# Kernel tuning notes

Hardware: AMD Instinct MI355X
Metric: run time of the kernel (lower is better)

## Reference

```python
import jax, jax.numpy as jnp
import numpy as np

N = 100000
E = 1600000
IN_C, HID_C, OUT_C = 128, 64, 16


def setup_inputs() -> dict:
    key = jax.random.key(0)
    k1, k2, k3, k4, k5 = jax.random.split(key, 5)
    x = jax.random.normal(k1, (N, IN_C), dtype=jnp.float32)
    edge_index = jax.random.randint(k2, (2, E), 0, N, dtype=jnp.int64)
    edge_weight = jax.random.uniform(k3, (E,), dtype=jnp.float32)
    # GCNConv weights (Glorot init, bias=False)
    W1 = jax.random.normal(k4, (IN_C, HID_C), dtype=jnp.float32) * (1.0 / np.sqrt(IN_C))
    W2 = jax.random.normal(k5, (HID_C, OUT_C), dtype=jnp.float32) * (1.0 / np.sqrt(HID_C))
    return {"x": x, "edge_index": edge_index, "edge_weight": edge_weight, "W1": W1, "W2": W2}


def _gcn_norm(edge_index, edge_weight, num_nodes):
    # add self loops with weight 1 (PyG gcn_norm with add_self_loops=True)
    loop = jnp.arange(num_nodes, dtype=edge_index.dtype)
    row = jnp.concatenate([edge_index[0], loop])
    col = jnpp_concat = jnp.concatenate([edge_index[1], loop])
    w = jnp.concatenate([edge_weight, jnp.ones((num_nodes,), edge_weight.dtype)])
    deg = jax.ops.segment_sum(w, col, num_segments=num_nodes)
    dinv = jnp.where(deg > 0, jax.lax.rsqrt(deg), 0.0)
    norm = dinv[row] * w * dinv[col]
    return row, col, norm


def _gcn_conv(x, W, row, col, norm, num_nodes):
    h = x @ W                              # [N, C_out] dense projection
    msg = h[row] * norm[:, None]           # gather + scale per edge
    return jax.ops.segment_sum(msg, col, num_segments=num_nodes)  # scatter-add at dst


def reference(x, edge_index, edge_weight, W1, W2):
    num_nodes = x.shape[0]
    row, col, norm = _gcn_norm(edge_index, edge_weight, num_nodes)
    h = _gcn_conv(x, W1, row, col, norm, num_nodes)
    h = jax.nn.relu(h)  # dropout_rate == 0 / eval -> identity
    h = _gcn_conv(h, W2, row, col, norm, num_nodes)
    return jax.nn.log_softmax(h, axis=1)
```

## Files before the change

### kernel.cpp

```cpp
#include <hip/hip_runtime.h>
#include <hip/hip_fp16.h>
#include <math.h>

constexpr int IN_C = 128, HID_C = 64, OUT_C = 16;
constexpr int BSH = 7;
constexpr int BCAP = 2560;
constexpr int REC_PT = BCAP / 256;
constexpr int TILE = 4096;
constexpr float WSC = 33554432.0f;

using f16x8 = __attribute__((ext_vector_type(8))) _Float16;
using f32x4 = __attribute__((ext_vector_type(4))) float;

__global__ __launch_bounds__(256) void k_hist(const int* __restrict__ col, int* __restrict__ histG,
                                              int E, int nb) {
  __shared__ int h[1024];
  int t = threadIdx.x, tile = blockIdx.x;
  for (int i = t; i < nb; i += 256) h[i] = 0;
  __syncthreads();
  int base = tile * TILE;
#pragma unroll
  for (int u = 0; u < TILE / 256; ++u) {
    int e = base + u * 256 + t;
    if (e < E) atomicAdd(&h[col[e] >> BSH], 1);
  }
  __syncthreads();
  for (int i = t; i < nb; i += 256) histG[(size_t)tile * nb + i] = h[i];
}

__global__ __launch_bounds__(256) void k_cscan(int* __restrict__ histG, int* __restrict__ btot,
                                               int T, int nb) {
  int b = blockIdx.x, t = threadIdx.x;
  __shared__ int s[512];
  int i0 = t, i1 = t + 256;
  s[i0] = (i0 < T) ? histG[(size_t)i0 * nb + b] : 0;
  s[i1] = (i1 < T) ? histG[(size_t)i1 * nb + b] : 0;
  __syncthreads();
  int c0 = s[i0], c1 = s[i1];
  for (int off = 1; off < 512; off <<= 1) {
    int a0 = (i0 >= off) ? s[i0 - off] : 0;
    int a1 = (i1 >= off) ? s[i1 - off] : 0;
    __syncthreads();
    s[i0] += a0; s[i1] += a1;
    __syncthreads();
  }
  if (i0 < T) histG[(size_t)i0 * nb + b] = s[i0] - c0;
  if (i1 < T) histG[(size_t)i1 * nb + b] = s[i1] - c1;
  if (t == 0) btot[b] = s[511];
}

__global__ __launch_bounds__(256) void k_scat2(const int* __restrict__ row, const int* __restrict__ col,
                                               const float* __restrict__ w, const int* __restrict__ histG,
                                               uint2* __restrict__ rec, int E, int nb) {
  __shared__ int soff[1024];
  int t = threadIdx.x, tile = blockIdx.x;
  for (int i = t; i < nb; i += 256) soff[i] = histG[(size_t)tile * nb + i];
  __syncthreads();
  int base = tile * TILE;
#pragma unroll
  for (int u = 0; u < TILE / 256; ++u) {
    int e = base + u * 256 + t;
    if (e < E) {
      int r = row[e], d = col[e];
      int b = d >> BSH;
      unsigned lo = (unsigned)(d & ((1 << BSH) - 1));
      unsigned wf = __float2uint_rn(w[e] * WSC);
      if (wf > 33554431u) wf = 33554431u;
      int slot = atomicAdd(&soff[b], 1);
      if (slot < BCAP)
        rec[(size_t)b * BCAP + slot] = make_uint2((unsigned)r, (lo << 25) | wf);
    }
  }
}

__global__ __launch_bounds__(256) void k_buck(const int* __restrict__ btot, const uint2* __restrict__ rec,
                                              int2* __restrict__ pairs, int* __restrict__ ptrg,
                                              int* __restrict__ cntg, float* __restrict__ dinvg,
                                              int n) {
  int b = blockIdx.x;
  int t = threadIdx.x;
  int cnt = btot[b];
  if (cnt > BCAP) cnt = BCAP;
  __shared__ int lcnt[128];
  __shared__ float lws[128];
  __shared__ int lptr[128];
  if (t < 128) { lcnt[t] = 0; lws[t] = 0.f; }
  __syncthreads();
  uint2 rv[REC_PT];
  int rk[REC_PT];
#pragma unroll
  for (int u = 0; u < REC_PT; ++u) {
    int i = u * 256 + t;
    if (i < cnt) {
      uint2 v = rec[(size_t)b * BCAP + i];
      rv[u] = v;
      int lo = v.y >> 25;
      rk[u] = atomicAdd(&lcnt[lo], 1);
      atomicAdd(&lws[lo], (float)(v.y & 0x1FFFFFFu) * (1.0f / WSC));
    }
  }
  __syncthreads();
  if (t < 128) lptr[t] = lcnt[t];
  __syncthreads();
  for (int off = 1; off < 128; off <<= 1) {
    int v = (t < 128 && t >= off) ? lptr[t - off] : 0;
    __syncthreads();
    if (t < 128 && t >= off) lptr[t] += v;
    __syncthreads();
  }
  if (t < 128) {
    int d = (b << BSH) + t;
    if (d < n) {
      ptrg[d] = b * BCAP + lptr[t] - lcnt[t];
      cntg[d] = lcnt[t];
      dinvg[d] = rsqrtf(1.0f + lws[t]);
    }
  }
#pragma unroll
  for (int u = 0; u < REC_PT; ++u) {
    int i = u * 256 + t;
    if (i < cnt) {
      uint2 v = rv[u];
      int lo = v.y >> 25;
      float wv = (float)(v.y & 0x1FFFFFFu) * (1.0f / WSC);
      pairs[(size_t)b * BCAP + (lptr[lo] - lcnt[lo]) + rk[u]] = make_int2((int)v.x, __float_as_int(wv));
    }
  }
}

__global__ __launch_bounds__(256) void k_gemm1(const float* __restrict__ x, const float* __restrict__ W1,
                                               const float* __restrict__ dinv,
                                               __half* __restrict__ h1h, int n) {
  __shared__ _Float16 w1t[HID_C][IN_C];
  int t = threadIdx.x;
  for (int i = t; i < IN_C * HID_C / 4; i += 256) {
    float4 v = ((const float4*)W1)[i];
    int k = (i * 4) / HID_C;
    int c = (i * 4) % HID_C;
    w1t[c + 0][k] = (_Float16)v.x;
    w1t[c + 1][k] = (_Float16)v.y;
    w1t[c + 2][k] = (_Float16)v.z;
    w1t[c + 3][k] = (_Float16)v.w;
  }
  __syncthreads();
  int wave = t >> 6, lane = t & 63;
  int row0 = (blockIdx.x * 4 + wave) * 16;
  if (row0 >= n) return;
  int lrow = lane & 15, lkg = lane >> 4;
  bool rvalid = (row0 + lrow) < n;
  const float* xr = x + (size_t)(row0 + lrow) * IN_C;
  f32x4 acc[4];
#pragma unroll
  for (int cg = 0; cg < 4; ++cg) acc[cg] = (f32x4){0.f, 0.f, 0.f, 0.f};
#pragma unroll
  for (int ks = 0; ks < 4; ++ks) {
    int k0 = ks * 32 + lkg * 8;
    f16x8 a;
    if (rvalid) {
      float4 u0 = *(const float4*)&xr[k0];
      float4 u1 = *(const float4*)&xr[k0 + 4];
      a[0] = (_Float16)u0.x; a[1] = (_Float16)u0.y; a[2] = (_Float16)u0.z; a[3] = (_Float16)u0.w;
      a[4] = (_Float16)u1.x; a[5] = (_Float16)u1.y; a[6] = (_Float16)u1.z; a[7] = (_Float16)u1.w;
    } else {
#pragma unroll
      for (int j = 0; j < 8; ++j) a[j] = (_Float16)0.f;
    }
#pragma unroll
    for (int cg = 0; cg < 4; ++cg) {
      f16x8 bfrag = *(const f16x8*)&w1t[cg * 16 + lrow][k0];
      acc[cg] = __builtin_amdgcn_mfma_f32_16x16x32_f16(a, bfrag, acc[cg], 0, 0, 0);
    }
  }
  float dv[4];
#pragma unroll
  for (int r = 0; r < 4; ++r) {
    int gr = row0 + lkg * 4 + r;
    dv[r] = (gr < n) ? dinv[gr] : 0.f;
  }
#pragma unroll
  for (int cg = 0; cg < 4; ++cg) {
#pragma unroll
    for (int r = 0; r < 4; ++r) {
      int gr = row0 + lkg * 4 + r;
      if (gr < n)
        h1h[(size_t)gr * HID_C + cg * 16 + lrow] = __float2half_rn(dv[r] * acc[cg][r]);
    }
  }
}

__global__ __launch_bounds__(256) void k_agg1f(const int* __restrict__ ptr, const int* __restrict__ cnt,
                                               const int2* __restrict__ pairs, const float* __restrict__ dinv,
                                               const __half* __restrict__ h1h, const float* __restrict__ W2,
                                               __half* __restrict__ h2h, int n) {
  __shared__ float w2s[HID_C * OUT_C];
  __shared__ float s[4][68];
  int t = threadIdx.x;
  ((float4*)w2s)[t] = ((const float4*)W2)[t];
  int wv = t >> 6, lane = t & 63;
  int d = blockIdx.x * 4 + wv;
  if (d < n) {
    d = __builtin_amdgcn_readfirstlane(d);
    int k = ptr[d], end = k + cnt[d];
    float dd = dinv[d];
    float acc = __half2float(h1h[(size_t)d * HID_C + lane]);
    for (; k + 8 <= end; k += 8) {
      int2 p[8];
      float v[8];
#pragma unroll
      for (int u = 0; u < 8; ++u) p[u] = pairs[k + u];
#pragma unroll
      for (int u = 0; u < 8; ++u)
        v[u] = __half2float(h1h[(size_t)p[u].x * HID_C + lane]);
#pragma unroll
      for (int u = 0; u < 8; ++u) acc = fmaf(__int_as_float(p[u].y), v[u], acc);
    }
    if (k + 4 <= end) {
      int2 p[4];
      float v[4];
#pragma unroll
      for (int u = 0; u < 4; ++u) p[u] = pairs[k + u];
#pragma unroll
      for (int u = 0; u < 4; ++u)
        v[u] = __half2float(h1h[(size_t)p[u].x * HID_C + lane]);
#pragma unroll
      for (int u = 0; u < 4; ++u) acc = fmaf(__int_as_float(p[u].y), v[u], acc);
      k += 4;
    }
    for (; k < end; ++k) {
      int2 p = pairs[k];
      acc = fmaf(__int_as_float(p.y), __half2float(h1h[(size_t)p.x * HID_C + lane]), acc);
    }
    s[wv][lane] = fmaxf(dd * acc, 0.f);
  } else {
    s[wv][lane] = 0.f;
  }
  __syncthreads();
  if (t < 64) {
    int nl = t >> 4, j = t & 15;
    int dn = blockIdx.x * 4 + nl;
    if (dn < n) {
      float a2 = 0.f;
#pragma unroll
      for (int c = 0; c < HID_C; ++c) a2 = fmaf(s[nl][c], w2s[c * OUT_C + j], a2);
      h2h[(size_t)dn * OUT_C + j] = __float2half_rn(dinv[dn] * a2);
    }
  }
}

__global__ __launch_bounds__(256) void k_agg2(const int* __restrict__ ptr, const int* __restrict__ cnt,
                                              const int2* __restrict__ pairs, const float* __restrict__ dinv,
                                              const __half* __restrict__ h2h, float* __restrict__ out, int n) {
  int t = threadIdx.x;
  int d = blockIdx.x * 16 + (t >> 4);
  if (d >= n) return;
  int j = t & 15;
  int k = ptr[d], end = k + cnt[d];
  float dd = dinv[d];
  float acc = __half2float(h2h[(size_t)d * OUT_C + j]);
  for (; k + 8 <= end; k += 8) {
    int2 p[8];
    float v[8];
#pragma unroll
    for (int u = 0; u < 8; ++u) p[u] = pairs[k + u];
#pragma unroll
    for (int u = 0; u < 8; ++u)
      v[u] = __half2float(h2h[(size_t)p[u].x * OUT_C + j]);
#pragma unroll
    for (int u = 0; u < 8; ++u) acc = fmaf(__int_as_float(p[u].y), v[u], acc);
  }
  if (k + 4 <= end) {
    int2 p[4];
    float v[4];
#pragma unroll
    for (int u = 0; u < 4; ++u) p[u] = pairs[k + u];
#pragma unroll
    for (int u = 0; u < 4; ++u)
      v[u] = __half2float(h2h[(size_t)p[u].x * OUT_C + j]);
#pragma unroll
    for (int u = 0; u < 4; ++u) acc = fmaf(__int_as_float(p[u].y), v[u], acc);
    k += 4;
  }
  for (; k < end; ++k) {
    int2 p = pairs[k];
    acc = fmaf(__int_as_float(p.y), __half2float(h2h[(size_t)p.x * OUT_C + j]), acc);
  }
  float lg = dd * acc;
  float mx = lg;
#pragma unroll
  for (int off = 8; off; off >>= 1) mx = fmaxf(mx, __shfl_xor(mx, off, 16));
  float sm = expf(lg - mx);
#pragma unroll
  for (int off = 8; off; off >>= 1) sm += __shfl_xor(sm, off, 16);
  out[(size_t)d * OUT_C + j] = lg - mx - logf(sm);
}

extern "C" void kernel_launch(void* const* d_in, const int* in_sizes, int n_in,
                              void* d_out, int out_size, void* d_ws, size_t ws_size,
                              hipStream_t stream) {
  const float* x  = (const float*)d_in[0];
  const int*   ei = (const int*)d_in[1];
  const float* ew = (const float*)d_in[2];
  const float* W1 = (const float*)d_in[3];
  const float* W2 = (const float*)d_in[4];
  const int N = in_sizes[0] / IN_C;
  const int E = in_sizes[2];
  const int* row = ei;
  const int* col = ei + E;
  float* out = (float*)d_out;
  const int NBUK = (N + (1 << BSH) - 1) >> BSH;
  const int T = (E + TILE - 1) / TILE;

  char* p = (char*)d_ws;
  int2*  pairs= (int2*)p;             p += (size_t)NBUK * BCAP * 8;
  int*   ptr  = (int*)p;              p += (size_t)N * 4;
  int*   cnt  = (int*)p;              p += (size_t)N * 4;
  float* dinv = (float*)p;            p += (size_t)N * 4;
  int*   histG= (int*)p;              p += (size_t)T * NBUK * 4;
  int*   btot = (int*)p;              p += (size_t)NBUK * 4;
  char*  uni  = p;                    p += (size_t)N * HID_C * 4;
  uint2* rec  = (uint2*)uni;
  __half* h1h = (__half*)uni;
  __half* h2h = (__half*)(uni + (size_t)N * HID_C * 2);

  dim3 b(256);
  k_hist <<<T, b, 0, stream>>>(col, histG, E, NBUK);
  k_cscan<<<NBUK, b, 0, stream>>>(histG, btot, T, NBUK);
  k_scat2<<<T, b, 0, stream>>>(row, col, ew, histG, rec, E, NBUK);
  k_buck <<<NBUK, b, 0, stream>>>(btot, rec, pairs, ptr, cnt, dinv, N);
  k_gemm1<<<(N + 63) / 64, b, 0, stream>>>(x, W1, dinv, h1h, N);
  k_agg1f<<<(N + 3) / 4, b, 0, stream>>>(ptr, cnt, pairs, dinv, h1h, W2, h2h, N);
  k_agg2 <<<(N + 15) / 16, b, 0, stream>>>(ptr, cnt, pairs, dinv, h2h, out, N);
}
```

Measured before the change: 162.1 us.

## Split edge lists across lane groups with vectorized half4 gathers in aggregations

Both aggregation kernels now give each wavefront one destination node. Groups of lanes process different edges in parallel, each lane loading 4 halfs at once, and the partial sums are combined with cross-lane shuffles. In agg2 this replaces 16-lane per-node mapping (16 nodes per block) with a full 64-lane wave per node (4 nodes per block), so each gather round covers 32 edges with fewer serial iterations per node. This aims to raise memory-level parallelism and cut loop trip counts on long neighbour lists. It costs shuffle reductions, clamped redundant loads in the tail iterations, and four times as many blocks for agg2.

```diff
diff --git a/kernel.cpp b/kernel.cpp
--- a/kernel.cpp
+++ b/kernel.cpp
@@ -10,6 +10,7 @@
 constexpr float WSC = 33554432.0f;
 
 using f16x8 = __attribute__((ext_vector_type(8))) _Float16;
+using f16x4 = __attribute__((ext_vector_type(4))) _Float16;
 using f32x4 = __attribute__((ext_vector_type(4))) float;
 
 __global__ __launch_bounds__(256) void k_hist(const int* __restrict__ col, int* __restrict__ histG,
@@ -193,46 +194,60 @@
                                                const __half* __restrict__ h1h, const float* __restrict__ W2,
                                                __half* __restrict__ h2h, int n) {
   __shared__ float w2s[HID_C * OUT_C];
-  __shared__ float s[4][68];
+  __shared__ __align__(16) float s[4][68];
   int t = threadIdx.x;
   ((float4*)w2s)[t] = ((const float4*)W2)[t];
+  __syncthreads();
   int wv = t >> 6, lane = t & 63;
+  int g = lane >> 4;
+  int c4 = (lane & 15) * 4;
   int d = blockIdx.x * 4 + wv;
   if (d < n) {
     d = __builtin_amdgcn_readfirstlane(d);
     int k = ptr[d], end = k + cnt[d];
     float dd = dinv[d];
-    float acc = __half2float(h1h[(size_t)d * HID_C + lane]);
-    for (; k + 8 <= end; k += 8) {
-      int2 p[8];
-      float v[8];
-#pragma unroll
-      for (int u = 0; u < 8; ++u) p[u] = pairs[k + u];
+    f32x4 acc = {0.f, 0.f, 0.f, 0.f};
+    if (g == 0) {
+      f16x4 sv = *(const f16x4*)&h1h[(size_t)d * HID_C + c4];
+      acc[0] = (float)sv[0]; acc[1] = (float)sv[1];
+      acc[2] = (float)sv[2]; acc[3] = (float)sv[3];
+    }
+    int last = end - 1;
+    for (; k < end; k += 32) {
+      int2 p[8]; float w[8]; f16x4 v[8];
+#pragma unroll
+      for (int u = 0; u < 8; ++u) {
+        int idx = k + u * 4 + g;
+        int ic = (idx <= last) ? idx : last;
+        p[u] = pairs[ic];
+        w[u] = (idx <= last) ? __int_as_float(p[u].y) : 0.f;
+      }
 #pragma unroll
       for (int u = 0; u < 8; ++u)
-        v[u] = __half2float(h1h[(size_t)p[u].x * HID_C + lane]);
-#pragma unroll
-      for (int u = 0; u < 8; ++u) acc = fmaf(__int_as_float(p[u].y), v[u], acc);
-    }
-    if (k + 4 <= end) {
-      int2 p[4];
-      float v[4];
-#pragma unroll
-      for (int u = 0; u < 4; ++u) p[u] = pairs[k + u];
-#pragma unroll
-      for (int u = 0; u < 4; ++u)
-        v[u] = __half2float(h1h[(size_t)p[u].x * HID_C + lane]);
-#pragma unroll
-      for (int u = 0; u < 4; ++u) acc = fmaf(__int_as_float(p[u].y), v[u], acc);
-      k += 4;
-    }
-    for (; k < end; ++k) {
-      int2 p = pairs[k];
-      acc = fmaf(__int_as_float(p.y), __half2float(h1h[(size_t)p.x * HID_C + lane]), acc);
-    }
-    s[wv][lane] = fmaxf(dd * acc, 0.f);
+        v[u] = *(const f16x4*)&h1h[(size_t)p[u].x * HID_C + c4];
+#pragma unroll
+      for (int u = 0; u < 8; ++u) {
+        acc[0] = fmaf(w[u], (float)v[u][0], acc[0]);
+        acc[1] = fmaf(w[u], (float)v[u][1], acc[1]);
+        acc[2] = fmaf(w[u], (float)v[u][2], acc[2]);
+        acc[3] = fmaf(w[u], (float)v[u][3], acc[3]);
+      }
+    }
+#pragma unroll
+    for (int i = 0; i < 4; ++i) {
+      acc[i] += __shfl_xor(acc[i], 16);
+      acc[i] += __shfl_xor(acc[i], 32);
+    }
+    if (g == 0) {
+      float4 r;
+      r.x = fmaxf(dd * acc[0], 0.f);
+      r.y = fmaxf(dd * acc[1], 0.f);
+      r.z = fmaxf(dd * acc[2], 0.f);
+      r.w = fmaxf(dd * acc[3], 0.f);
+      *(float4*)&s[wv][c4] = r;
+    }
   } else {
-    s[wv][lane] = 0.f;
+    if (g == 0) *(float4*)&s[wv][c4] = make_float4(0.f, 0.f, 0.f, 0.f);
   }
   __syncthreads();
   if (t < 64) {
@@ -251,47 +266,64 @@
                                               const int2* __restrict__ pairs, const float* __restrict__ dinv,
                                               const __half* __restrict__ h2h, float* __restrict__ out, int n) {
   int t = threadIdx.x;
-  int d = blockIdx.x * 16 + (t >> 4);
+  int wv = t >> 6, lane = t & 63;
+  int d = blockIdx.x * 4 + wv;
   if (d >= n) return;
-  int j = t & 15;
+  d = __builtin_amdgcn_readfirstlane(d);
+  int sl = lane >> 2;
+  int j4 = (lane & 3) * 4;
   int k = ptr[d], end = k + cnt[d];
   float dd = dinv[d];
-  float acc = __half2float(h2h[(size_t)d * OUT_C + j]);
-  for (; k + 8 <= end; k += 8) {
-    int2 p[8];
-    float v[8];
-#pragma unroll
-    for (int u = 0; u < 8; ++u) p[u] = pairs[k + u];
-#pragma unroll
-    for (int u = 0; u < 8; ++u)
-      v[u] = __half2float(h2h[(size_t)p[u].x * OUT_C + j]);
-#pragma unroll
-    for (int u = 0; u < 8; ++u) acc = fmaf(__int_as_float(p[u].y), v[u], acc);
-  }
-  if (k + 4 <= end) {
-    int2 p[4];
-    float v[4];
-#pragma unroll
-    for (int u = 0; u < 4; ++u) p[u] = pairs[k + u];
-#pragma unroll
-    for (int u = 0; u < 4; ++u)
-      v[u] = __half2float(h2h[(size_t)p[u].x * OUT_C + j]);
-#pragma unroll
-    for (int u = 0; u < 4; ++u) acc = fmaf(__int_as_float(p[u].y), v[u], acc);
-    k += 4;
-  }
-  for (; k < end; ++k) {
-    int2 p = pairs[k];
-    acc = fmaf(__int_as_float(p.y), __half2float(h2h[(size_t)p.x * OUT_C + j]), acc);
-  }
-  float lg = dd * acc;
-  float mx = lg;
-#pragma unroll
-  for (int off = 8; off; off >>= 1) mx = fmaxf(mx, __shfl_xor(mx, off, 16));
-  float sm = expf(lg - mx);
-#pragma unroll
-  for (int off = 8; off; off >>= 1) sm += __shfl_xor(sm, off, 16);
-  out[(size_t)d * OUT_C + j] = lg - mx - logf(sm);
+  f32x4 acc = {0.f, 0.f, 0.f, 0.f};
+  if (sl == 0) {
+    f16x4 sv = *(const f16x4*)&h2h[(size_t)d * OUT_C + j4];
+    acc[0] = (float)sv[0]; acc[1] = (float)sv[1];
+    acc[2] = (float)sv[2]; acc[3] = (float)sv[3];
+  }
+  int last = end - 1;
+  for (; k < end; k += 32) {
+    int2 p[2]; float w[2]; f16x4 v[2];
+#pragma unroll
+    for (int u = 0; u < 2; ++u) {
+      int idx = k + u * 16 + sl;
+      int ic = (idx <= last) ? idx : last;
+      p[u] = pairs[ic];
+      w[u] = (idx <= last) ? __int_as_float(p[u].y) : 0.f;
+    }
+#pragma unroll
+    for (int u = 0; u < 2; ++u)
+      v[u] = *(const f16x4*)&h2h[(size_t)p[u].x * OUT_C + j4];
+#pragma unroll
+    for (int u = 0; u < 2; ++u) {
+      acc[0] = fmaf(w[u], (float)v[u][0], acc[0]);
+      acc[1] = fmaf(w[u], (float)v[u][1], acc[1]);
+      acc[2] = fmaf(w[u], (float)v[u][2], acc[2]);
+      acc[3] = fmaf(w[u], (float)v[u][3], acc[3]);
+    }
+  }
+#pragma unroll
+  for (int i = 0; i < 4; ++i) {
+    acc[i] += __shfl_xor(acc[i], 4);
+    acc[i] += __shfl_xor(acc[i], 8);
+    acc[i] += __shfl_xor(acc[i], 16);
+    acc[i] += __shfl_xor(acc[i], 32);
+  }
+  float lg[4];
+#pragma unroll
+  for (int i = 0; i < 4; ++i) lg[i] = dd * acc[i];
+  float mx = fmaxf(fmaxf(lg[0], lg[1]), fmaxf(lg[2], lg[3]));
+  mx = fmaxf(mx, __shfl_xor(mx, 1));
+  mx = fmaxf(mx, __shfl_xor(mx, 2));
+  float sm = expf(lg[0] - mx) + expf(lg[1] - mx) + expf(lg[2] - mx) + expf(lg[3] - mx);
+  sm += __shfl_xor(sm, 1);
+  sm += __shfl_xor(sm, 2);
+  float ls = logf(sm);
+  if (sl == 0) {
+    float4 r;
+    r.x = lg[0] - mx - ls; r.y = lg[1] - mx - ls;
+    r.z = lg[2] - mx - ls; r.w = lg[3] - mx - ls;
+    *(float4*)&out[(size_t)d * OUT_C + j4] = r;
+  }
 }
 
 extern "C" void kernel_launch(void* const* d_in, const int* in_sizes, int n_in,
@@ -329,5 +361,5 @@
   k_buck <<<NBUK, b, 0, stream>>>(btot, rec, pairs, ptr, cnt, dinv, N);
   k_gemm1<<<(N + 63) / 64, b, 0, stream>>>(x, W1, dinv, h1h, N);
   k_agg1f<<<(N + 3) / 4, b, 0, stream>>>(ptr, cnt, pairs, dinv, h1h, W2, h2h, N);
-  k_agg2 <<<(N + 15) / 16, b, 0, stream>>>(ptr, cnt, pairs, dinv, h2h, out, N);
-}
+  k_agg2 <<<(N + 3) / 4, b, 0, stream>>>(ptr, cnt, pairs, dinv, h2h, out, N);
+}
```

Result: slower. 171.1 us (+5.6%).
